# Kernel optimization log

Measured on AMD Instinct MI355X. Metric: run time of the kernel, lower is better.

## Reference

```python
import jax, jax.numpy as jnp
import numpy as np

B, N, D = 4, 1024, 1024
H, HD, G = 16, 64, 4          # num_heads, dim_heads, num_groups
KVH = H // G                   # kv heads = 4


def setup_inputs() -> dict:
    key = jax.random.key(0)
    ks = jax.random.split(key, 5)
    s = 0.02
    return {
        "x": jax.random.normal(ks[0], (B, N, D), jnp.float32),
        "Wq": jax.random.normal(ks[1], (D, H * HD), jnp.float32) * s,
        "Wkv": jax.random.normal(ks[2], (D, 2 * H * HD // G), jnp.float32) * s,
        "Wg": jax.random.normal(ks[3], (D, H * HD), jnp.float32) * s,
        "bg": jnp.zeros((H * HD,), jnp.float32),
        "Wo": jax.random.normal(ks[4], (H * HD, D), jnp.float32) * s,
    }


def reference(x, Wq, Wkv, Wg, bg, Wo):
    # QKV projections (no bias on q/kv/o; bias on gate)
    q = (x @ Wq).reshape(B, N, H, HD).transpose(0, 2, 1, 3)        # (B,H,N,HD)
    kv = x @ Wkv                                                    # (B,N,2*KVH*HD)
    k, v = jnp.split(kv, 2, axis=-1)
    k = k.reshape(B, N, KVH, HD).transpose(0, 2, 1, 3)             # (B,KVH,N,HD)
    v = v.reshape(B, N, KVH, HD).transpose(0, 2, 1, 3)
    # GQA: repeat_interleave kv heads to match query heads
    k = jnp.repeat(k, G, axis=1)                                    # (B,H,N,HD)
    v = jnp.repeat(v, G, axis=1)
    # scaled dot product attention
    scores = jnp.einsum("bhqd,bhkd->bhqk", q, k) / jnp.sqrt(jnp.float32(HD))
    attn = jax.nn.softmax(scores, axis=-1)
    out = jnp.einsum("bhqk,bhkd->bhqd", attn, v)                    # (B,H,N,HD)
    out = out.transpose(0, 2, 1, 3).reshape(B, N, H * HD)
    # elementwise gate then output projection
    gate = x @ Wg + bg
    return (gate * out) @ Wo
```

## Files before the change

kernel.cpp:

```cpp
#include <hip/hip_runtime.h>
#include <hip/hip_bf16.h>
#include <stdint.h>

#define BB 4
#define NN 1024
#define DD 1024
#define HH 16
#define HDIM 64
#define KVHH 4
#define MM (BB * NN)

typedef __hip_bfloat16 bf16;
typedef __attribute__((ext_vector_type(8))) short bf16x8;
typedef __attribute__((ext_vector_type(4))) short bf16x4;
typedef __attribute__((ext_vector_type(4))) float f32x4;

__device__ __forceinline__ float b2f(unsigned short u) {
  return __uint_as_float(((unsigned)u) << 16);
}
__device__ __forceinline__ unsigned short f2b(float x) {
  bf16 h = __float2bfloat16(x);
  unsigned short u;
  __builtin_memcpy(&u, &h, 2);
  return u;
}
__device__ __forceinline__ f32x4 mfma16(bf16x8 a, bf16x8 b, f32x4 c) {
  return __builtin_amdgcn_mfma_f32_16x16x32_bf16(a, b, c, 0, 0, 0);
}
__device__ __forceinline__ f32x4 mfma16k16(bf16x4 a, bf16x4 b, f32x4 c) {
#if __has_builtin(__builtin_amdgcn_mfma_f32_16x16x16bf16_1k)
  return __builtin_amdgcn_mfma_f32_16x16x16bf16_1k(a, b, c, 0, 0, 0);
#else
  asm("s_nop 1\n\tv_mfma_f32_16x16x16_bf16 %0, %1, %2, %0"
      : "+v"(c)
      : "v"(a), "v"(b));
  return c;
#endif
}
__device__ __forceinline__ bf16x4 vlo(bf16x8 v) {
  return __builtin_shufflevector(v, v, 0, 1, 2, 3);
}
__device__ __forceinline__ bf16x4 vhi(bf16x8 v) {
  return __builtin_shufflevector(v, v, 4, 5, 6, 7);
}
__device__ __forceinline__ void gl_lds16(const short* g, short* l) {
  __builtin_amdgcn_global_load_lds(
      (const __attribute__((address_space(1))) unsigned*)g,
      (__attribute__((address_space(3))) unsigned*)l, 16, 0, 0);
}

__global__ __launch_bounds__(256) void transpose_all(
    const float* __restrict__ Wq, const float* __restrict__ Wkv,
    const float* __restrict__ Wg, const float* __restrict__ Wo,
    const float* __restrict__ bg, const float* __restrict__ x,
    short* __restrict__ WcT, short* __restrict__ WoT,
    float* __restrict__ bias, short* __restrict__ xb) {
  const int z = blockIdx.z;
  if (z == 4) {
    if (blockIdx.y == 0 && blockIdx.x < 10) {
      int i = blockIdx.x * 256 + threadIdx.x;
      if (i < 2560) bias[i] = (i >= 1024 && i < 2048) ? bg[i - 1024] : 0.f;
    }
    return;
  }
  if (z == 5) {
    int base = (blockIdx.y * 16 + blockIdx.x) * 256 + threadIdx.x;
#pragma unroll
    for (int it = 0; it < 16; ++it) {
      int i = base + it * 65536;
      float4 v = *(const float4*)&x[(size_t)i * 4];
      ushort4 o;
      o.x = f2b(v.x); o.y = f2b(v.y); o.z = f2b(v.z); o.w = f2b(v.w);
      *(ushort4*)&xb[(size_t)i * 4] = o;
    }
    return;
  }
  const float* W;
  short* WT;
  int N = 1024;
  const int K = 1024;
  if (z == 0) { W = Wq; WT = WcT; }
  else if (z == 1) { W = Wg; WT = WcT + 1048576; }
  else if (z == 2) {
    W = Wkv; WT = WcT + 2097152; N = 512;
    if (blockIdx.x >= 8) return;
  } else { W = Wo; WT = WoT; }

  __shared__ short T[64 * 68];
  const int tid = threadIdx.x;
  const int n0 = blockIdx.x * 64, k0 = blockIdx.y * 64;
  {
    int i0 = tid >> 4, j4 = (tid & 15) * 4;
#pragma unroll
    for (int ii = 0; ii < 4; ++ii) {
      int i = i0 + 16 * ii;
      float4 w = *(const float4*)&W[(size_t)(k0 + i) * N + n0 + j4];
      ushort4 o;
      o.x = f2b(w.x); o.y = f2b(w.y); o.z = f2b(w.z); o.w = f2b(w.w);
      *(ushort4*)&T[i * 68 + j4] = o;
    }
  }
  __syncthreads();
  {
    int n = tid >> 2, k16 = (tid & 3) * 16;
    short tmp[16];
#pragma unroll
    for (int kk = 0; kk < 16; ++kk) tmp[kk] = T[(k16 + kk) * 68 + n];
    short* dst = WT + (size_t)(n0 + n) * K + k0 + k16;
#pragma unroll
    for (int s = 0; s < 16; s += 4) *(ushort4*)&dst[s] = *(const ushort4*)&tmp[s];
  }
}

__global__ __launch_bounds__(256, 3) void gemm_proj(
    const short* __restrict__ A, const short* __restrict__ WT,
    const float* __restrict__ bias, short* __restrict__ qc,
    short* __restrict__ gc, short* __restrict__ kc, short* __restrict__ vt) {
  __shared__ short As[2][128 * 32];
  __shared__ short Bs[2][128 * 32];
  const int tid = threadIdx.x;
  const int wave = tid >> 6, lane = tid & 63, l15 = lane & 15, quad = lane >> 4;
  const int bid0 = blockIdx.x + blockIdx.y * 20;
  const int swz = (bid0 & 7) * 80 + (bid0 >> 3);
  const int bx = swz % 20, by = swz / 20;
  const int m0 = by * 128, n0 = bx * 128;
  const int wm = (wave & 1) * 64, wn = (wave >> 1) * 64;
  const int arow = tid >> 2, ac = (tid & 3) * 8;
  const short* asrc = A + (size_t)(m0 + arow) * 1024 + ac;
  const short* bsrc = WT + (size_t)(n0 + arow) * 1024 + ac;

  gl_lds16(asrc, &As[0][wave * 512]);
  gl_lds16(asrc + 64 * 1024, &As[0][2048 + wave * 512]);
  gl_lds16(bsrc, &Bs[0][wave * 512]);
  gl_lds16(bsrc + 64 * 1024, &Bs[0][2048 + wave * 512]);

  f32x4 acc[4][4] = {};
  for (int k = 0; k < 32; ++k) {
    const int cur = k & 1;
    __syncthreads();
    if (k < 31) {
      const short* ap = asrc + (k + 1) * 32;
      const short* bp = bsrc + (k + 1) * 32;
      gl_lds16(ap, &As[1 - cur][wave * 512]);
      gl_lds16(ap + 64 * 1024, &As[1 - cur][2048 + wave * 512]);
      gl_lds16(bp, &Bs[1 - cur][wave * 512]);
      gl_lds16(bp + 64 * 1024, &Bs[1 - cur][2048 + wave * 512]);
    }
    bf16x8 af[4], bfr[4];
#pragma unroll
    for (int i = 0; i < 4; ++i)
      af[i] = *(const bf16x8*)&As[cur][(wm + 16 * i + l15) * 32 + quad * 8];
#pragma unroll
    for (int j = 0; j < 4; ++j)
      bfr[j] = *(const bf16x8*)&Bs[cur][(wn + 16 * j + l15) * 32 + quad * 8];
#pragma unroll
    for (int i = 0; i < 4; ++i)
#pragma unroll
      for (int j = 0; j < 4; ++j) acc[i][j] = mfma16(af[i], bfr[j], acc[i][j]);
  }

  const int reg = (n0 + wn) >> 6;
  if (reg < 16) {
#pragma unroll
    for (int j = 0; j < 4; ++j) {
      int d = 16 * j + l15;
#pragma unroll
      for (int i = 0; i < 4; ++i)
#pragma unroll
        for (int r = 0; r < 4; ++r) {
          int row = m0 + wm + 16 * i + quad * 4 + r;
          int b = row >> 10, tok = row & 1023;
          ((unsigned short*)qc)[((size_t)((b * 16 + reg) * 1024 + tok)) * 64 + d] =
              f2b(acc[i][j][r] * 0.18033688f);
        }
    }
  } else if (reg < 32) {
#pragma unroll
    for (int j = 0; j < 4; ++j) {
      int d = 16 * j + l15;
      float bv = bias[n0 + wn + d];
#pragma unroll
      for (int i = 0; i < 4; ++i)
#pragma unroll
        for (int r = 0; r < 4; ++r) {
          int row = m0 + wm + 16 * i + quad * 4 + r;
          int b = row >> 10, tok = row & 1023;
          ((unsigned short*)gc)[((size_t)((b * 16 + reg - 16) * 1024 + tok)) * 64 + d] =
              f2b(acc[i][j][r] + bv);
        }
    }
  } else if (reg < 36) {
    int kvh = reg - 32;
#pragma unroll
    for (int j = 0; j < 4; ++j) {
      int d = 16 * j + l15;
      int dh = d >> 5, dq = (d >> 3) & 3, di = d & 7;
#pragma unroll
      for (int i = 0; i < 4; ++i)
#pragma unroll
        for (int r = 0; r < 4; ++r) {
          int row = m0 + wm + 16 * i + quad * 4 + r;
          int b = row >> 10, tok = row & 1023;
          int kt = tok >> 6, kh = (tok >> 5) & 1, k32 = tok & 31;
          int ksub = k32 >> 4, kl = k32 & 15;
          size_t koff = (size_t)(b * 4 + kvh) * 65536 +
                        (size_t)((kt * 2 + kh) * 2048 + (ksub * 2 + dh) * 512 +
                                 (dq * 16 + kl) * 8 + di);
          ((unsigned short*)kc)[koff] = f2b(acc[i][j][r]);
        }
    }
  } else {
    int kvh = reg - 36;
#pragma unroll
    for (int j = 0; j < 4; ++j) {
      int dt = j;
#pragma unroll
      for (int i = 0; i < 4; ++i) {
        int row0 = m0 + wm + 16 * i + quad * 4;
        int b = row0 >> 10, tok0 = row0 & 1023;
        int kt = tok0 >> 6, kh = (tok0 >> 5) & 1, isub = (tok0 >> 4) & 1;
        size_t voff = (size_t)(b * 4 + kvh) * 65536 +
                      (size_t)((kt * 2 + kh) * 2048 + (isub * 2 + (dt >> 1)) * 512 +
                               (quad * 16 + l15) * 8 + (dt & 1) * 4);
        ushort4 o;
        o.x = f2b(acc[i][j][0]);
        o.y = f2b(acc[i][j][1]);
        o.z = f2b(acc[i][j][2]);
        o.w = f2b(acc[i][j][3]);
        *(ushort4*)&((unsigned short*)vt)[voff] = o;
      }
    }
  }
}

__global__ __launch_bounds__(256, 4) void gemm_out(
    const short* __restrict__ A, const short* __restrict__ WT,
    float* __restrict__ Cout) {
  __shared__ short As[2][2][64 * 32];
  __shared__ short Bs[2][2][64 * 32];
  const int tid = threadIdx.x;
  const int wave = tid >> 6, lane = tid & 63, l15 = lane & 15, quad = lane >> 4;
  const int bid0 = blockIdx.x + blockIdx.y * 16;
  const int swz = (bid0 & 7) * 128 + (bid0 >> 3);
  const int m0 = (swz >> 4) * 64, n0 = (swz & 15) * 64;
  const int wm = (wave & 1) * 32, wn = (wave >> 1) * 32;
  const int arow = tid >> 2, ac = (tid & 3) * 8;
  const short* asrc = A + (size_t)(m0 + arow) * 1024 + ac;
  const short* bsrc = WT + (size_t)(n0 + arow) * 1024 + ac;

  gl_lds16(asrc, &As[0][0][wave * 512]);
  gl_lds16(asrc + 32, &As[0][1][wave * 512]);
  gl_lds16(bsrc, &Bs[0][0][wave * 512]);
  gl_lds16(bsrc + 32, &Bs[0][1][wave * 512]);

  f32x4 acc[2][2] = {};
  for (int k = 0; k < 16; ++k) {
    const int cur = k & 1;
    __syncthreads();
    if (k < 15) {
      const short* ap = asrc + (k + 1) * 64;
      const short* bp = bsrc + (k + 1) * 64;
      gl_lds16(ap, &As[1 - cur][0][wave * 512]);
      gl_lds16(ap + 32, &As[1 - cur][1][wave * 512]);
      gl_lds16(bp, &Bs[1 - cur][0][wave * 512]);
      gl_lds16(bp + 32, &Bs[1 - cur][1][wave * 512]);
    }
#pragma unroll
    for (int s = 0; s < 2; ++s) {
      bf16x8 af[2], bfr[2];
#pragma unroll
      for (int i = 0; i < 2; ++i)
        af[i] = *(const bf16x8*)&As[cur][s][(wm + 16 * i + l15) * 32 + quad * 8];
#pragma unroll
      for (int j = 0; j < 2; ++j)
        bfr[j] = *(const bf16x8*)&Bs[cur][s][(wn + 16 * j + l15) * 32 + quad * 8];
#pragma unroll
      for (int i = 0; i < 2; ++i)
#pragma unroll
        for (int j = 0; j < 2; ++j) acc[i][j] = mfma16(af[i], bfr[j], acc[i][j]);
    }
  }
#pragma unroll
  for (int j = 0; j < 2; ++j) {
    int col = n0 + wn + 16 * j + l15;
#pragma unroll
    for (int i = 0; i < 2; ++i) {
#pragma unroll
      for (int r = 0; r < 4; ++r) {
        int row = m0 + wm + 16 * i + quad * 4 + r;
        Cout[(size_t)row * 1024 + col] = acc[i][j][r];
      }
    }
  }
}

__global__ __launch_bounds__(256, 4) void attn_mfma15(
    const short* __restrict__ qc, const short* __restrict__ gc,
    const short* __restrict__ kc, const short* __restrict__ vt,
    unsigned short* __restrict__ gated) {
  __shared__ short KV[2][8192];
  __shared__ float Lpart[4 * 32];
  __shared__ float Lq[64];
  float* OA = (float*)&KV[0][0];
  float* OB = OA + 64 * 33;
  const int tid = threadIdx.x;
  const int w = tid >> 6, lane = tid & 63, l15 = lane & 15, quad = lane >> 4;
  const int qh = w >> 1, kh = w & 1;
  const int bid0 = blockIdx.x + blockIdx.y * 16;
  const int swz = (bid0 & 7) * 128 + (bid0 >> 3);
  const int qt = swz & 15, bh = swz >> 4;
  const int b = bh >> 4, h = bh & 15, kvh = h >> 2;

  bf16x8 qf[2][2];
#pragma unroll
  for (int jq = 0; jq < 2; ++jq) {
    const short* qp = qc + ((size_t)((b * 16 + h) * 1024) + qt * 64 + qh * 32 +
                            16 * jq + l15) * 64 + quad * 8;
    qf[jq][0] = *(const bf16x8*)qp;
    qf[jq][1] = *(const bf16x8*)(qp + 32);
  }

  const short* kbase = kc + (size_t)(b * 4 + kvh) * 65536;
  const short* vbase = vt + (size_t)(b * 4 + kvh) * 65536;
  const int wdst = w * 512;

#define STAGE(CUR, KT)                                                         \
  {                                                                            \
    const short* ks = kbase + (size_t)(KT) * 4096;                             \
    const short* vs = vbase + (size_t)(KT) * 4096;                             \
    gl_lds16(ks + tid * 8, &KV[CUR][wdst]);                                    \
    gl_lds16(ks + 2048 + tid * 8, &KV[CUR][2048 + wdst]);                      \
    gl_lds16(vs + tid * 8, &KV[CUR][4096 + wdst]);                             \
    gl_lds16(vs + 2048 + tid * 8, &KV[CUR][6144 + wdst]);                      \
  }

  f32x4 oacc[2][4] = {};
  float ls[2] = {0.f, 0.f};

#define EXPPV8(ST, JQ, WA, WB)                                                 \
  {                                                                            \
    float p0 = exp2f((ST)[0]), p1 = exp2f((ST)[1]);                            \
    float p2 = exp2f((ST)[2]), p3 = exp2f((ST)[3]);                            \
    ls[JQ] += (p0 + p1) + (p2 + p3);                                           \
    bf16x4 pbf;                                                                \
    pbf[0] = (short)f2b(p0);                                                   \
    pbf[1] = (short)f2b(p1);                                                   \
    pbf[2] = (short)f2b(p2);                                                   \
    pbf[3] = (short)f2b(p3);                                                   \
    oacc[JQ][0] = mfma16k16(vlo(WA), pbf, oacc[JQ][0]);                        \
    oacc[JQ][1] = mfma16k16(vhi(WA), pbf, oacc[JQ][1]);                        \
    oacc[JQ][2] = mfma16k16(vlo(WB), pbf, oacc[JQ][2]);                        \
    oacc[JQ][3] = mfma16k16(vhi(WB), pbf, oacc[JQ][3]);                        \
  }

  STAGE(0, 0);
  for (int kt = 0; kt < 16; ++kt) {
    const int cur = kt & 1;
    __syncthreads();
    if (kt < 15) STAGE(cur ^ 1, kt + 1);
    const short* kl = &KV[cur][kh * 2048 + lane * 8];
    const short* vl = &KV[cur][4096 + kh * 2048 + lane * 8];
    bf16x8 kA0 = *(const bf16x8*)(kl);
    bf16x8 kA1 = *(const bf16x8*)(kl + 512);
    bf16x8 kA2 = *(const bf16x8*)(kl + 1024);
    bf16x8 kA3 = *(const bf16x8*)(kl + 1536);
    bf16x8 w0 = *(const bf16x8*)(vl);
    bf16x8 w1 = *(const bf16x8*)(vl + 512);
    bf16x8 w2 = *(const bf16x8*)(vl + 1024);
    bf16x8 w3 = *(const bf16x8*)(vl + 1536);
    f32x4 s00 = mfma16(kA0, qf[0][0], (f32x4){0.f, 0.f, 0.f, 0.f});
    s00 = mfma16(kA1, qf[0][1], s00);
    f32x4 s10 = mfma16(kA0, qf[1][0], (f32x4){0.f, 0.f, 0.f, 0.f});
    s10 = mfma16(kA1, qf[1][1], s10);
    EXPPV8(s00, 0, w0, w1);
    EXPPV8(s10, 1, w0, w1);
    f32x4 s01 = mfma16(kA2, qf[0][0], (f32x4){0.f, 0.f, 0.f, 0.f});
    s01 = mfma16(kA3, qf[0][1], s01);
    f32x4 s11 = mfma16(kA2, qf[1][0], (f32x4){0.f, 0.f, 0.f, 0.f});
    s11 = mfma16(kA3, qf[1][1], s11);
    EXPPV8(s01, 0, w2, w3);
    EXPPV8(s11, 1, w2, w3);
  }
#undef EXPPV8
#undef STAGE

#pragma unroll
  for (int jq = 0; jq < 2; ++jq) {
    ls[jq] += __shfl_xor(ls[jq], 16);
    ls[jq] += __shfl_xor(ls[jq], 32);
  }
  __syncthreads();
  if (quad == 0) {
#pragma unroll
    for (int jq = 0; jq < 2; ++jq) Lpart[w * 32 + 16 * jq + l15] = ls[jq];
  }
  float* Ob = qh ? OB : OA;
  if (kh == 0) {
#pragma unroll
    for (int jq = 0; jq < 2; ++jq)
#pragma unroll
      for (int dt = 0; dt < 4; ++dt)
#pragma unroll
        for (int r = 0; r < 4; ++r)
          Ob[(16 * dt + 4 * quad + r) * 33 + 16 * jq + l15] = oacc[jq][dt][r];
  }
  __syncthreads();
  if (kh == 1) {
#pragma unroll
    for (int jq = 0; jq < 2; ++jq)
#pragma unroll
      for (int dt = 0; dt < 4; ++dt)
#pragma unroll
        for (int r = 0; r < 4; ++r)
          Ob[(16 * dt + 4 * quad + r) * 33 + 16 * jq + l15] += oacc[jq][dt][r];
  }
  if (tid < 64) {
    int ql = tid & 31, qh2 = tid >> 5;
    Lq[tid] = Lpart[qh2 * 64 + ql] + Lpart[qh2 * 64 + 32 + ql];
  }
  __syncthreads();

  const int d = 16 * w + l15;
#pragma unroll
  for (int jq = 0; jq < 4; ++jq) {
    const float* Osrc = (jq < 2) ? OA : OB;
#pragma unroll
    for (int r = 0; r < 4; ++r) {
      int qloc = 16 * jq + 4 * quad + r;
      float ov = Osrc[d * 33 + (qloc & 31)];
      float lv = Lq[qloc];
      float gv = b2f(((const unsigned short*)gc)[
          ((size_t)((b * 16 + h) * 1024) + qt * 64 + qloc) * 64 + d]);
      size_t row = (size_t)(b * NN + qt * 64 + qloc);
      gated[row * 1024 + h * 64 + d] = f2b(ov / lv * gv);
    }
  }
}

extern "C" void kernel_launch(void* const* d_in, const int* in_sizes, int n_in,
                              void* d_out, int out_size, void* d_ws,
                              size_t ws_size, hipStream_t stream) {
  const float* x = (const float*)d_in[0];
  const float* Wq = (const float*)d_in[1];
  const float* Wkv = (const float*)d_in[2];
  const float* Wg = (const float*)d_in[3];
  const float* bg = (const float*)d_in[4];
  const float* Wo = (const float*)d_in[5];
  float* out = (float*)d_out;

  short* ws = (short*)d_ws;
  short* xb = ws;
  short* WcT = xb + 4194304;
  short* WoT = WcT + 2621440;
  short* qc = WoT + 1048576;
  short* gc = qc + 4194304;
  short* kc = gc + 4194304;
  short* vtw = kc + 1048576;
  float* bias_f32 = (float*)(vtw + 1048576);

  dim3 blk(256);
  transpose_all<<<dim3(16, 16, 6), blk, 0, stream>>>(Wq, Wkv, Wg, Wo, bg, x,
                                                     WcT, WoT, bias_f32, xb);
  gemm_proj<<<dim3(20, 32), blk, 0, stream>>>(xb, WcT, bias_f32, qc, gc, kc, vtw);
  attn_mfma15<<<dim3(16, 64), blk, 0, stream>>>(qc, gc, kc, vtw, (unsigned short*)xb);
  gemm_out<<<dim3(16, 64), blk, 0, stream>>>(xb, WoT, out);
}
```

Measured before the change: 167.6 us.

## Double attention query tile to 128 rows per block for more K/V reuse

Each attention block now handles 128 queries instead of 64, with each wave holding four 16-row query fragments, so every K/V tile loaded into shared memory is reused across twice as many queries. The grid is halved, launch bounds drop to 2 blocks per SM, and the output reduction buffer moves to a dedicated shared array instead of aliasing the K/V buffer. This cuts K/V global traffic and staging per query at the cost of more registers, more shared memory, and half as many blocks to fill the GPU.

```diff
diff --git a/kernel.cpp b/kernel.cpp
--- a/kernel.cpp
+++ b/kernel.cpp
@@ -294,27 +294,26 @@
   }
 }
 
-__global__ __launch_bounds__(256, 4) void attn_mfma15(
+__global__ __launch_bounds__(256, 2) void attn_mfma16(
     const short* __restrict__ qc, const short* __restrict__ gc,
     const short* __restrict__ kc, const short* __restrict__ vt,
     unsigned short* __restrict__ gated) {
   __shared__ short KV[2][8192];
-  __shared__ float Lpart[4 * 32];
-  __shared__ float Lq[64];
-  float* OA = (float*)&KV[0][0];
-  float* OB = OA + 64 * 33;
+  __shared__ float Obuf[2 * 64 * 65];
+  __shared__ float Lpart[4 * 64];
+  __shared__ float Lq[128];
   const int tid = threadIdx.x;
   const int w = tid >> 6, lane = tid & 63, l15 = lane & 15, quad = lane >> 4;
   const int qh = w >> 1, kh = w & 1;
-  const int bid0 = blockIdx.x + blockIdx.y * 16;
-  const int swz = (bid0 & 7) * 128 + (bid0 >> 3);
-  const int qt = swz & 15, bh = swz >> 4;
+  const int bid0 = blockIdx.x + blockIdx.y * 8;
+  const int swz = (bid0 & 7) * 64 + (bid0 >> 3);
+  const int qt = swz & 7, bh = swz >> 3;
   const int b = bh >> 4, h = bh & 15, kvh = h >> 2;
 
-  bf16x8 qf[2][2];
-#pragma unroll
-  for (int jq = 0; jq < 2; ++jq) {
-    const short* qp = qc + ((size_t)((b * 16 + h) * 1024) + qt * 64 + qh * 32 +
+  bf16x8 qf[4][2];
+#pragma unroll
+  for (int jq = 0; jq < 4; ++jq) {
+    const short* qp = qc + ((size_t)((b * 16 + h) * 1024) + qt * 128 + qh * 64 +
                             16 * jq + l15) * 64 + quad * 8;
     qf[jq][0] = *(const bf16x8*)qp;
     qf[jq][1] = *(const bf16x8*)(qp + 32);
@@ -334,8 +333,8 @@
     gl_lds16(vs + 2048 + tid * 8, &KV[CUR][6144 + wdst]);                      \
   }
 
-  f32x4 oacc[2][4] = {};
-  float ls[2] = {0.f, 0.f};
+  f32x4 oacc[4][4] = {};
+  float ls[4] = {0.f, 0.f, 0.f, 0.f};
 
 #define EXPPV8(ST, JQ, WA, WB)                                                 \
   {                                                                            \
@@ -368,70 +367,70 @@
     bf16x8 w1 = *(const bf16x8*)(vl + 512);
     bf16x8 w2 = *(const bf16x8*)(vl + 1024);
     bf16x8 w3 = *(const bf16x8*)(vl + 1536);
-    f32x4 s00 = mfma16(kA0, qf[0][0], (f32x4){0.f, 0.f, 0.f, 0.f});
-    s00 = mfma16(kA1, qf[0][1], s00);
-    f32x4 s10 = mfma16(kA0, qf[1][0], (f32x4){0.f, 0.f, 0.f, 0.f});
-    s10 = mfma16(kA1, qf[1][1], s10);
-    EXPPV8(s00, 0, w0, w1);
-    EXPPV8(s10, 1, w0, w1);
-    f32x4 s01 = mfma16(kA2, qf[0][0], (f32x4){0.f, 0.f, 0.f, 0.f});
-    s01 = mfma16(kA3, qf[0][1], s01);
-    f32x4 s11 = mfma16(kA2, qf[1][0], (f32x4){0.f, 0.f, 0.f, 0.f});
-    s11 = mfma16(kA3, qf[1][1], s11);
-    EXPPV8(s01, 0, w2, w3);
-    EXPPV8(s11, 1, w2, w3);
+#pragma unroll
+    for (int jq = 0; jq < 4; ++jq) {
+      f32x4 st = mfma16(kA0, qf[jq][0], (f32x4){0.f, 0.f, 0.f, 0.f});
+      st = mfma16(kA1, qf[jq][1], st);
+      EXPPV8(st, jq, w0, w1);
+    }
+#pragma unroll
+    for (int jq = 0; jq < 4; ++jq) {
+      f32x4 st = mfma16(kA2, qf[jq][0], (f32x4){0.f, 0.f, 0.f, 0.f});
+      st = mfma16(kA3, qf[jq][1], st);
+      EXPPV8(st, jq, w2, w3);
+    }
   }
 #undef EXPPV8
 #undef STAGE
 
 #pragma unroll
-  for (int jq = 0; jq < 2; ++jq) {
+  for (int jq = 0; jq < 4; ++jq) {
     ls[jq] += __shfl_xor(ls[jq], 16);
     ls[jq] += __shfl_xor(ls[jq], 32);
   }
-  __syncthreads();
   if (quad == 0) {
 #pragma unroll
-    for (int jq = 0; jq < 2; ++jq) Lpart[w * 32 + 16 * jq + l15] = ls[jq];
-  }
-  float* Ob = qh ? OB : OA;
+    for (int jq = 0; jq < 4; ++jq) Lpart[w * 64 + 16 * jq + l15] = ls[jq];
+  }
+
+  float* Ob = Obuf + qh * (64 * 65);
   if (kh == 0) {
 #pragma unroll
-    for (int jq = 0; jq < 2; ++jq)
+    for (int jq = 0; jq < 4; ++jq)
 #pragma unroll
       for (int dt = 0; dt < 4; ++dt)
 #pragma unroll
         for (int r = 0; r < 4; ++r)
-          Ob[(16 * dt + 4 * quad + r) * 33 + 16 * jq + l15] = oacc[jq][dt][r];
+          Ob[(16 * dt + 4 * quad + r) * 65 + 16 * jq + l15] = oacc[jq][dt][r];
   }
   __syncthreads();
   if (kh == 1) {
 #pragma unroll
-    for (int jq = 0; jq < 2; ++jq)
+    for (int jq = 0; jq < 4; ++jq)
 #pragma unroll
       for (int dt = 0; dt < 4; ++dt)
 #pragma unroll
         for (int r = 0; r < 4; ++r)
-          Ob[(16 * dt + 4 * quad + r) * 33 + 16 * jq + l15] += oacc[jq][dt][r];
-  }
-  if (tid < 64) {
-    int ql = tid & 31, qh2 = tid >> 5;
-    Lq[tid] = Lpart[qh2 * 64 + ql] + Lpart[qh2 * 64 + 32 + ql];
+          Ob[(16 * dt + 4 * quad + r) * 65 + 16 * jq + l15] += oacc[jq][dt][r];
+  }
+  if (tid < 128) {
+    int ql = tid & 63, qh2 = tid >> 6;
+    Lq[tid] = Lpart[qh2 * 128 + ql] + Lpart[qh2 * 128 + 64 + ql];
   }
   __syncthreads();
 
   const int d = 16 * w + l15;
 #pragma unroll
-  for (int jq = 0; jq < 4; ++jq) {
-    const float* Osrc = (jq < 2) ? OA : OB;
+  for (int jq = 0; jq < 8; ++jq) {
+    const float* Osrc = Obuf + (jq < 4 ? 0 : 64 * 65);
 #pragma unroll
     for (int r = 0; r < 4; ++r) {
       int qloc = 16 * jq + 4 * quad + r;
-      float ov = Osrc[d * 33 + (qloc & 31)];
+      float ov = Osrc[d * 65 + (qloc & 63)];
       float lv = Lq[qloc];
       float gv = b2f(((const unsigned short*)gc)[
-          ((size_t)((b * 16 + h) * 1024) + qt * 64 + qloc) * 64 + d]);
-      size_t row = (size_t)(b * NN + qt * 64 + qloc);
+          ((size_t)((b * 16 + h) * 1024) + qt * 128 + qloc) * 64 + d]);
+      size_t row = (size_t)(b * NN + qt * 128 + qloc);
       gated[row * 1024 + h * 64 + d] = f2b(ov / lv * gv);
     }
   }
@@ -462,6 +461,6 @@
   transpose_all<<<dim3(16, 16, 6), blk, 0, stream>>>(Wq, Wkv, Wg, Wo, bg, x,
                                                      WcT, WoT, bias_f32, xb);
   gemm_proj<<<dim3(20, 32), blk, 0, stream>>>(xb, WcT, bias_f32, qc, gc, kc, vtw);
-  attn_mfma15<<<dim3(16, 64), blk, 0, stream>>>(qc, gc, kc, vtw, (unsigned short*)xb);
+  attn_mfma16<<<dim3(8, 64), blk, 0, stream>>>(qc, gc, kc, vtw, (unsigned short*)xb);
   gemm_out<<<dim3(16, 64), blk, 0, stream>>>(xb, WoT, out);
 }
```

Result: slower. 171.4 us (+2.3%).

## Triple-buffer projection GEMM loads with partial vmcnt waits

Applied to the files above, without the earlier changes.

The projection GEMM moves from a double-buffered to a triple-buffered LDS pipeline, prefetching two K-steps ahead. Each iteration waits with s_waitcnt vmcnt(4), so only the current stage's global-to-LDS loads must finish, and a raw s_barrier replaces __syncthreads. This is meant to hide more global memory latency behind the MFMA work. LDS use grows from 32KB to 48KB per block, which may limit occupancy under the 3-blocks-per-CU launch bound, and correctness now depends on the vmcnt counting being exact.

```diff
diff --git a/kernel.cpp b/kernel.cpp
--- a/kernel.cpp
+++ b/kernel.cpp
@@ -116,8 +116,8 @@
     const short* __restrict__ A, const short* __restrict__ WT,
     const float* __restrict__ bias, short* __restrict__ qc,
     short* __restrict__ gc, short* __restrict__ kc, short* __restrict__ vt) {
-  __shared__ short As[2][128 * 32];
-  __shared__ short Bs[2][128 * 32];
+  __shared__ short As[3][128 * 32];
+  __shared__ short Bs[3][128 * 32];
   const int tid = threadIdx.x;
   const int wave = tid >> 6, lane = tid & 63, l15 = lane & 15, quad = lane >> 4;
   const int bid0 = blockIdx.x + blockIdx.y * 20;
@@ -129,23 +129,29 @@
   const short* asrc = A + (size_t)(m0 + arow) * 1024 + ac;
   const short* bsrc = WT + (size_t)(n0 + arow) * 1024 + ac;
 
-  gl_lds16(asrc, &As[0][wave * 512]);
-  gl_lds16(asrc + 64 * 1024, &As[0][2048 + wave * 512]);
-  gl_lds16(bsrc, &Bs[0][wave * 512]);
-  gl_lds16(bsrc + 64 * 1024, &Bs[0][2048 + wave * 512]);
+#define PSTAGE(BUF, K)                                                         \
+  {                                                                            \
+    const short* ap = asrc + (K)*32;                                           \
+    const short* bp = bsrc + (K)*32;                                           \
+    gl_lds16(ap, &As[BUF][wave * 512]);                                        \
+    gl_lds16(ap + 64 * 1024, &As[BUF][2048 + wave * 512]);                     \
+    gl_lds16(bp, &Bs[BUF][wave * 512]);                                        \
+    gl_lds16(bp + 64 * 1024, &Bs[BUF][2048 + wave * 512]);                     \
+  }
+
+  PSTAGE(0, 0);
+  PSTAGE(1, 1);
 
   f32x4 acc[4][4] = {};
   for (int k = 0; k < 32; ++k) {
-    const int cur = k & 1;
-    __syncthreads();
-    if (k < 31) {
-      const short* ap = asrc + (k + 1) * 32;
-      const short* bp = bsrc + (k + 1) * 32;
-      gl_lds16(ap, &As[1 - cur][wave * 512]);
-      gl_lds16(ap + 64 * 1024, &As[1 - cur][2048 + wave * 512]);
-      gl_lds16(bp, &Bs[1 - cur][wave * 512]);
-      gl_lds16(bp + 64 * 1024, &Bs[1 - cur][2048 + wave * 512]);
-    }
+    const int cur = k % 3;
+    if (k < 31)
+      asm volatile("s_waitcnt vmcnt(4)" ::: "memory");
+    else
+      asm volatile("s_waitcnt vmcnt(0)" ::: "memory");
+    __builtin_amdgcn_s_barrier();
+    __builtin_amdgcn_sched_barrier(0);
+    if (k < 30) PSTAGE((k + 2) % 3, k + 2);
     bf16x8 af[4], bfr[4];
 #pragma unroll
     for (int i = 0; i < 4; ++i)
@@ -158,6 +164,7 @@
 #pragma unroll
       for (int j = 0; j < 4; ++j) acc[i][j] = mfma16(af[i], bfr[j], acc[i][j]);
   }
+#undef PSTAGE
 
   const int reg = (n0 + wn) >> 6;
   if (reg < 16) {
```

New measurement: 169.8 us. Within noise of the previous version (+1.3%).
